# Optimization experiments

Hardware: AMD Instinct MI355X
Metric: run time of the kernel (lower is better)

The kernel has to match this reference:

```python
import jax, jax.numpy as jnp
import numpy as np

H, D_MODEL, D_K, D_V = 8, 512, 64, 64
B, S = 8, 2048


def setup_inputs() -> dict:
    key = jax.random.key(0)
    ks = jax.random.split(key, 11)
    scale = 1.0 / np.sqrt(D_MODEL)
    inp = {
        "q": jax.random.normal(ks[0], (B, S, D_MODEL), dtype=jnp.float32),
        "k": jax.random.normal(ks[1], (B, S, D_MODEL), dtype=jnp.float32),
        "v": jax.random.normal(ks[2], (B, S, D_MODEL), dtype=jnp.float32),
        # stacked per-head linear weights, [h, d_model, d_k/d_v] (in x out layout)
        "Wq": jax.random.normal(ks[3], (H, D_MODEL, D_K), dtype=jnp.float32) * scale,
        "bq": jax.random.normal(ks[4], (H, D_K), dtype=jnp.float32) * 0.01,
        "Wk": jax.random.normal(ks[5], (H, D_MODEL, D_K), dtype=jnp.float32) * scale,
        "bk": jax.random.normal(ks[6], (H, D_K), dtype=jnp.float32) * 0.01,
        "Wv": jax.random.normal(ks[7], (H, D_MODEL, D_V), dtype=jnp.float32) * scale,
        "bv": jax.random.normal(ks[8], (H, D_V), dtype=jnp.float32) * 0.01,
        "Wo": jax.random.normal(ks[9], (H * D_V, D_MODEL), dtype=jnp.float32) * (1.0 / np.sqrt(H * D_V)),
        "bo": jax.random.normal(ks[10], (D_MODEL,), dtype=jnp.float32) * 0.01,
    }
    return inp


def reference(q, k, v, Wq, bq, Wk, bk, Wv, bv, Wo, bo):
    # Per-head projections, vectorized over heads: [b, h, s, d_k]
    qh = jnp.einsum("bsd,hdk->bhsk", q, Wq) + bq[None, :, None, :]
    kh = jnp.einsum("bsd,hdk->bhsk", k, Wk) + bk[None, :, None, :]
    vh = jnp.einsum("bsd,hdv->bhsv", v, Wv) + bv[None, :, None, :]
    # scaled dot product: [b, h, s_q, s_k]
    scores = jnp.einsum("bhqd,bhkd->bhqk", qh, kh) / jnp.sqrt(jnp.float32(D_K))
    # NOTE: original applies softmax over dim=1 of [b, s_q, s_k] == the QUERY axis
    attn = jax.nn.softmax(scores, axis=2)
    ctx = jnp.einsum("bhqk,bhkv->bhqv", attn, vh)  # [b, h, s, d_v]
    # concat heads along feature dim (matches torch.cat(attentions, dim=2))
    concat = jnp.transpose(ctx, (0, 2, 1, 3)).reshape(ctx.shape[0], ctx.shape[2], H * D_V)
    return concat @ Wo + bo
```

## Files before the change

### kernel.cpp

```cpp
#include <hip/hip_runtime.h>
#include <hip/hip_bf16.h>
#include <math.h>

#define BB 8
#define SS 2048
#define HH 8
#define DM 512
#define DK 64

typedef short bf16x8 __attribute__((ext_vector_type(8)));
typedef float f32x4 __attribute__((ext_vector_type(4)));

static __device__ __forceinline__ short f2bf(float f) {
    union { __hip_bfloat16 h; short s; } u;
    u.h = __float2bfloat16(f);
    return u.s;
}

static __device__ __forceinline__ float fexp2(float x) {
#if __has_builtin(__builtin_amdgcn_exp2f)
    return __builtin_amdgcn_exp2f(x);
#else
    return __expf(x * 0.69314718056f);
#endif
}

static __device__ __forceinline__ void gld16(void* lds, const void* g) {
    __builtin_amdgcn_global_load_lds((const __attribute__((address_space(1))) void*)g,
                                     (__attribute__((address_space(3))) void*)lds, 16, 0, 0);
}

static __device__ __forceinline__ bf16x8 fragRow(const short* lds, int row, int cshort) {
    return *(const bf16x8*)(lds + row * 64 + (cshort ^ ((row & 7) << 3)));
}

static __device__ __forceinline__ void bar() {
    __builtin_amdgcn_s_barrier();
    __builtin_amdgcn_sched_barrier(0);
}
#define WAITV4 asm volatile("s_waitcnt vmcnt(4)" ::: "memory")
#define WAITV2 asm volatile("s_waitcnt vmcnt(2)" ::: "memory")
#define WAITV0 asm volatile("s_waitcnt vmcnt(0)" ::: "memory")
#define WAITL0 asm volatile("s_waitcnt lgkmcnt(0)" ::: "memory")
#define SCHED0 __builtin_amdgcn_sched_barrier(0)

__global__ __launch_bounds__(256) void tcvt(const float* __restrict__ src, short* __restrict__ dst,
                                            int R, int C) {
    __shared__ short T[64][72];
    const int r0 = blockIdx.x * 64, c0 = blockIdx.y * 64;
    const int t = threadIdx.x;
#pragma unroll
    for (int p = 0; p < 4; ++p) {
        int idx = t + 256 * p;
        int row = idx >> 4, c4 = (idx & 15) * 4;
        float4 v = *(const float4*)(src + (size_t)(r0 + row) * C + c0 + c4);
        T[c4 + 0][row] = f2bf(v.x);
        T[c4 + 1][row] = f2bf(v.y);
        T[c4 + 2][row] = f2bf(v.z);
        T[c4 + 3][row] = f2bf(v.w);
    }
    __syncthreads();
#pragma unroll
    for (int p = 0; p < 2; ++p) {
        int idx = t + 256 * p;
        int row = idx >> 3, slot = idx & 7;
        *(bf16x8*)(dst + (size_t)(c0 + row) * R + r0 + slot * 8) = *(const bf16x8*)&T[row][slot * 8];
    }
}

__global__ __launch_bounds__(256) void tcvt3(const float* __restrict__ Wq, const float* __restrict__ Wk,
                                             const float* __restrict__ Wv, short* __restrict__ WqT,
                                             short* __restrict__ WkT, short* __restrict__ WvT) {
    __shared__ short T[64][72];
    const int z = blockIdx.z;
    const int which = z >> 3, h = z & 7;
    const float* src = (which == 0 ? Wq : (which == 1 ? Wk : Wv)) + (size_t)h * DM * DK;
    short* dst = (which == 0 ? WqT : (which == 1 ? WkT : WvT)) + (size_t)h * DK * DM;
    const int r0 = blockIdx.x * 64;
    const int t = threadIdx.x;
#pragma unroll
    for (int p = 0; p < 4; ++p) {
        int idx = t + 256 * p;
        int row = idx >> 4, c4 = (idx & 15) * 4;
        float4 v = *(const float4*)(src + (size_t)(r0 + row) * DK + c4);
        T[c4 + 0][row] = f2bf(v.x);
        T[c4 + 1][row] = f2bf(v.y);
        T[c4 + 2][row] = f2bf(v.z);
        T[c4 + 3][row] = f2bf(v.w);
    }
    __syncthreads();
#pragma unroll
    for (int p = 0; p < 2; ++p) {
        int idx = t + 256 * p;
        int row = idx >> 3, slot = idx & 7;
        *(bf16x8*)(dst + (size_t)row * DM + r0 + slot * 8) = *(const bf16x8*)&T[row][slot * 8];
    }
}

__global__ __launch_bounds__(256, 4) void proj_mfma(const float* __restrict__ qX,
                                                    const float* __restrict__ kX,
                                                    const float* __restrict__ vX,
                                                    const short* __restrict__ WqT,
                                                    const short* __restrict__ WkT,
                                                    const short* __restrict__ WvT,
                                                    const float* __restrict__ bq,
                                                    const float* __restrict__ bk,
                                                    const float* __restrict__ bv,
                                                    short* __restrict__ qY,
                                                    short* __restrict__ kY,
                                                    short* __restrict__ vY,
                                                    float qscale) {
    __shared__ short As[128 * 64];
    __shared__ short Bs[2][64 * 64];
    const int mode = blockIdx.y;
    const float* X = mode == 0 ? qX : (mode == 1 ? kX : vX);
    const short* WT = mode == 0 ? WqT : (mode == 1 ? WkT : WvT);
    const float* bias = mode == 0 ? bq : (mode == 1 ? bk : bv);
    short* Y = mode == 0 ? qY : (mode == 1 ? kY : vY);
    const float scale = mode == 0 ? qscale : 1.0f;

    const int lin = blockIdx.x;
    const int b = lin & 7, h = (lin >> 3) & 7;
    const int s0 = (lin >> 6) * 128;
    const int bh = b * 8 + h;
    const int t = threadIdx.x;
    const int l = t & 63, w = t >> 6;
    const int lr = l & 15, g = l >> 4;
    const float* Xb = X + ((size_t)b * SS + s0) * DM;
    const short* Wh = WT + (size_t)h * DK * DM;
    f32x4 acc[2][4];
#pragma unroll
    for (int i = 0; i < 2; ++i)
#pragma unroll
        for (int j = 0; j < 4; ++j) acc[i][j] = (f32x4){0.f, 0.f, 0.f, 0.f};

    float4 ra[8];
    auto loadA = [&](int k0) {
#pragma unroll
        for (int p = 0; p < 4; ++p) {
            int c = p * 256 + t;
            int row = c >> 3, col = (c & 7) * 8;
            ra[2 * p]     = *(const float4*)(Xb + (size_t)row * DM + k0 + col);
            ra[2 * p + 1] = *(const float4*)(Xb + (size_t)row * DM + k0 + col + 4);
        }
    };
    auto writeA = [&]() {
#pragma unroll
        for (int p = 0; p < 4; ++p) {
            int c = p * 256 + t;
            int row = c >> 3, slot = c & 7;
            bf16x8 o;
            o[0] = f2bf(ra[2 * p].x); o[1] = f2bf(ra[2 * p].y);
            o[2] = f2bf(ra[2 * p].z); o[3] = f2bf(ra[2 * p].w);
            o[4] = f2bf(ra[2 * p + 1].x); o[5] = f2bf(ra[2 * p + 1].y);
            o[6] = f2bf(ra[2 * p + 1].z); o[7] = f2bf(ra[2 * p + 1].w);
            *(bf16x8*)(As + row * 64 + ((slot ^ (row & 7)) * 8)) = o;
        }
    };
    auto stageB = [&](int buf, int k0) {
#pragma unroll
        for (int p = 0; p < 2; ++p) {
            int c = p * 256 + w * 64 + l;
            int row = c >> 3, slot = c & 7;
            gld16(Bs[buf] + (size_t)(p * 256 + w * 64) * 8,
                  Wh + (size_t)row * DM + k0 + ((slot ^ (row & 7)) * 8));
        }
    };

    loadA(0);
    stageB(0, 0);
    writeA();
    __syncthreads();
    int cur = 0;
    for (int k0 = 0; k0 < DM; k0 += 64) {
        const bool next = (k0 + 64 < DM);
        if (next) { loadA(k0 + 64); stageB(cur ^ 1, k0 + 64); }
        SCHED0;
        bf16x8 bfr[4][2];
#pragma unroll
        for (int bf = 0; bf < 4; ++bf) {
            bfr[bf][0] = fragRow(Bs[cur], 16 * bf + lr, 8 * g);
            bfr[bf][1] = fragRow(Bs[cur], 16 * bf + lr, 32 + 8 * g);
        }
#pragma unroll
        for (int af = 0; af < 2; ++af) {
            bf16x8 a0 = fragRow(As, 32 * w + 16 * af + lr, 8 * g);
            bf16x8 a1 = fragRow(As, 32 * w + 16 * af + lr, 32 + 8 * g);
#pragma unroll
            for (int bf = 0; bf < 4; ++bf) {
                acc[af][bf] = __builtin_amdgcn_mfma_f32_16x16x32_bf16(a0, bfr[bf][0], acc[af][bf], 0, 0, 0);
                acc[af][bf] = __builtin_amdgcn_mfma_f32_16x16x32_bf16(a1, bfr[bf][1], acc[af][bf], 0, 0, 0);
            }
        }
        if (next) {
            bar();
            writeA();
            __syncthreads();
        }
        cur ^= 1;
    }
    if (mode == 2) {
        short* Yb = Y + (size_t)bh * DK * SS;
#pragma unroll
        for (int qf = 0; qf < 2; ++qf)
#pragma unroll
            for (int nf = 0; nf < 4; ++nf) {
                int n = 16 * nf + lr;
                float bv2 = bias[h * DK + n];
                short4 o;
                o.x = f2bf(acc[qf][nf][0] + bv2);
                o.y = f2bf(acc[qf][nf][1] + bv2);
                o.z = f2bf(acc[qf][nf][2] + bv2);
                o.w = f2bf(acc[qf][nf][3] + bv2);
                *(short4*)(Yb + (size_t)n * SS + s0 + 32 * w + 8 * g + 4 * qf) = o;
            }
    } else {
        short* Yb = Y + ((size_t)bh * SS + s0) * DK;
#pragma unroll
        for (int qf = 0; qf < 2; ++qf)
#pragma unroll
            for (int nf = 0; nf < 4; ++nf) {
                int n = 16 * nf + lr;
                float bv2 = bias[h * DK + n];
#pragma unroll
                for (int r = 0; r < 4; ++r)
                    Yb[(size_t)(32 * w + 16 * qf + 4 * g + r) * DK + n] =
                        f2bf((acc[qf][nf][r] + bv2) * scale);
            }
    }
}

__global__ __launch_bounds__(256, 4) void stats_mfma(const short* __restrict__ qs,
                                                     const short* __restrict__ kh,
                                                     float* __restrict__ izOut) {
    __shared__ short LDS[16384];
    const int bid = blockIdx.x;
    const int r = bid & 63;
    const int bh = ((r & 7) << 3) | (r >> 3);
    const int k0 = (bid >> 6) * 256;
    const int t = threadIdx.x;
    const int l = t & 63, w = t >> 6;
    const int lr = l & 15, g = l >> 4;
    const short* Qb = qs + (size_t)bh * SS * DK;
    const short* Kb = kh + ((size_t)bh * SS + k0) * DK;

#pragma unroll
    for (int p = 0; p < 8; ++p) {
        int c = p * 256 + w * 64 + l;
        int row = c >> 3, slot = c & 7;
        gld16(LDS + (size_t)(p * 256 + w * 64) * 8,
              Kb + (size_t)row * DK + ((slot ^ (row & 7)) * 8));
    }
    WAITV0;
    bar();
    bf16x8 bk[4][2];
#pragma unroll
    for (int c2 = 0; c2 < 4; ++c2) {
        bk[c2][0] = fragRow(LDS, 64 * w + 16 * c2 + lr, 8 * g);
        bk[c2][1] = fragRow(LDS, 64 * w + 16 * c2 + lr, 32 + 8 * g);
    }
    WAITL0;
    SCHED0;
    bar();

    auto stageQ = [&](int buf, int qq) {
#pragma unroll
        for (int p = 0; p < 2; ++p) {
            int c = p * 256 + w * 64 + l;
            int row = c >> 3, slot = c & 7;
            gld16(LDS + buf * 4096 + (size_t)(p * 256 + w * 64) * 8,
                  Qb + (size_t)(qq + row) * DK + ((slot ^ (row & 7)) * 8));
        }
    };
    stageQ(0, 0);
    stageQ(1, 64);
    WAITV2;
    bar();

    f32x4 zacc[4];
#pragma unroll
    for (int c2 = 0; c2 < 4; ++c2) zacc[c2] = (f32x4){0.f, 0.f, 0.f, 0.f};

    int cur = 0;
    for (int it = 0; it < 32; ++it) {
        const bool pre = (it < 30);
        if (pre) stageQ((cur + 2) & 3, (it + 2) * 64);
        const short* Qcur = LDS + cur * 4096;
        __builtin_amdgcn_s_setprio(1);
#pragma unroll
        for (int qf = 0; qf < 4; ++qf) {
            bf16x8 aq0 = fragRow(Qcur, 16 * qf + lr, 8 * g);
            bf16x8 aq1 = fragRow(Qcur, 16 * qf + lr, 32 + 8 * g);
#pragma unroll
            for (int c2 = 0; c2 < 4; ++c2) {
                f32x4 s = {0.f, 0.f, 0.f, 0.f};
                s = __builtin_amdgcn_mfma_f32_16x16x32_bf16(aq0, bk[c2][0], s, 0, 0, 0);
                s = __builtin_amdgcn_mfma_f32_16x16x32_bf16(aq1, bk[c2][1], s, 0, 0, 0);
#pragma unroll
                for (int rr = 0; rr < 4; ++rr)
                    zacc[c2][rr] += fexp2(s[rr]);
            }
        }
        __builtin_amdgcn_s_setprio(0);
        if (pre) { WAITV2; } else { WAITV0; }
        bar();
        cur = (cur + 1) & 3;
    }
#pragma unroll
    for (int c2 = 0; c2 < 4; ++c2) {
        float z = zacc[c2][0] + zacc[c2][1] + zacc[c2][2] + zacc[c2][3];
        z += __shfl_xor(z, 16);
        z += __shfl_xor(z, 32);
        if (l < 16)
            izOut[(size_t)bh * SS + k0 + 64 * w + 16 * c2 + l] = 1.f / z;
    }
}

__global__ __launch_bounds__(256, 2) void ctx_mfma(const short* __restrict__ qs,
                                                   const short* __restrict__ kh,
                                                   const short* __restrict__ vP,
                                                   const float* __restrict__ izArr,
                                                   short* __restrict__ ctxc) {
    __shared__ short LDS[24576];
    const int bid = blockIdx.x;
    const int r = bid & 63;
    const int bh = ((r & 7) << 3) | (r >> 3);
    const int q0 = (bid >> 6) * 256;
    const int b = bh >> 3, h = bh & 7;
    const int t = threadIdx.x;
    const int l = t & 63, w = t >> 6;
    const int lr = l & 15, g = l >> 4;
    const short* Qb = qs + ((size_t)bh * SS + q0) * DK;
    const short* Kb = kh + (size_t)bh * SS * DK;
    const short* Vb = vP + (size_t)bh * DK * SS;
    const float* zB = izArr + (size_t)bh * SS;

#pragma unroll
    for (int p = 0; p < 8; ++p) {
        int c = p * 256 + w * 64 + l;
        int row = c >> 3, slot = c & 7;
        gld16(LDS + (size_t)(p * 256 + w * 64) * 8,
              Qb + (size_t)row * DK + ((slot ^ (row & 7)) * 8));
    }
    WAITV0;
    bar();
    bf16x8 qfr[4][2];
#pragma unroll
    for (int qf = 0; qf < 4; ++qf)
#pragma unroll
        for (int c = 0; c < 2; ++c)
            qfr[qf][c] = fragRow(LDS, 64 * w + 16 * qf + lr, 32 * c + 8 * g);
    WAITL0;
    SCHED0;
    bar();

    auto stageKV = [&](int buf, int kk) {
#pragma unroll
        for (int p = 0; p < 2; ++p) {
            int c = p * 256 + w * 64 + l;
            int row = c >> 3, slot = c & 7;
            gld16(LDS + buf * 4096 + (size_t)(p * 256 + w * 64) * 8,
                  Kb + (size_t)(kk + row) * DK + ((slot ^ (row & 7)) * 8));
        }
#pragma unroll
        for (int p = 0; p < 2; ++p) {
            int c = p * 256 + w * 64 + l;
            int row = c >> 3, slot = c & 7;
            gld16(LDS + 12288 + buf * 4096 + (size_t)(p * 256 + w * 64) * 8,
                  Vb + (size_t)row * SS + kk + ((slot ^ (row & 7)) * 8));
        }
    };
    stageKV(0, 0);
    stageKV(1, 64);
    WAITV4;
    bar();

    f32x4 acc[4][4];
#pragma unroll
    for (int a = 0; a < 4; ++a)
#pragma unroll
        for (int b2 = 0; b2 < 4; ++b2) acc[a][b2] = (f32x4){0.f, 0.f, 0.f, 0.f};

    int cur = 0;
    for (int it = 0; it < 32; ++it) {
        const int k0 = it * 64;
        const bool pre = (it < 30);
        f32x4 z4[4];
#pragma unroll
        for (int kf = 0; kf < 4; ++kf)
            z4[kf] = *(const f32x4*)(zB + k0 + 16 * kf + 4 * g);
        SCHED0;
        if (pre) {
            int nb = cur + 2; if (nb >= 3) nb -= 3;
            stageKV(nb, k0 + 128);
        }
        const short* Kcur = LDS + cur * 4096;
        const short* Vcur = LDS + 12288 + cur * 4096;
        __builtin_amdgcn_s_setprio(1);
        bf16x8 Kf[4][2];
#pragma unroll
        for (int kf = 0; kf < 4; ++kf) {
            Kf[kf][0] = fragRow(Kcur, 16 * kf + lr, 8 * g);
            Kf[kf][1] = fragRow(Kcur, 16 * kf + lr, 32 + 8 * g);
        }
        bf16x8 pa[4][2];
#pragma unroll
        for (int qf = 0; qf < 4; ++qf) {
            float pw[4][4];
#pragma unroll
            for (int kf = 0; kf < 4; ++kf) {
                f32x4 s = {0.f, 0.f, 0.f, 0.f};
                s = __builtin_amdgcn_mfma_f32_16x16x32_bf16(Kf[kf][0], qfr[qf][0], s, 0, 0, 0);
                s = __builtin_amdgcn_mfma_f32_16x16x32_bf16(Kf[kf][1], qfr[qf][1], s, 0, 0, 0);
#pragma unroll
                for (int rr = 0; rr < 4; ++rr)
                    pw[kf][rr] = fexp2(s[rr]) * z4[kf][rr];
            }
#pragma unroll
            for (int c = 0; c < 2; ++c)
#pragma unroll
                for (int e = 0; e < 4; ++e) {
                    pa[qf][c][e]     = f2bf(pw[2 * c][e]);
                    pa[qf][c][4 + e] = f2bf(pw[2 * c + 1][e]);
                }
        }
#pragma unroll
        for (int vf = 0; vf < 4; ++vf)
#pragma unroll
            for (int c = 0; c < 2; ++c) {
                bf16x8 bv2 = fragRow(Vcur, 16 * vf + lr, 32 * c + 8 * g);
#pragma unroll
                for (int qf = 0; qf < 4; ++qf)
                    acc[qf][vf] = __builtin_amdgcn_mfma_f32_16x16x32_bf16(pa[qf][c], bv2, acc[qf][vf], 0, 0, 0);
            }
        __builtin_amdgcn_s_setprio(0);
        if (pre) { WAITV4; } else { WAITV0; }
        bar();
        cur = (cur == 2) ? 0 : cur + 1;
    }
    short* Cb = ctxc + ((size_t)b * SS + q0) * (HH * DK) + h * DK;
#pragma unroll
    for (int qf = 0; qf < 4; ++qf)
#pragma unroll
        for (int vf = 0; vf < 4; ++vf)
#pragma unroll
            for (int rr = 0; rr < 4; ++rr)
                Cb[(size_t)(64 * w + 16 * qf + 4 * g + rr) * (HH * DK) + 16 * vf + lr] =
                    f2bf(acc[qf][vf][rr]);
}

__global__ __launch_bounds__(256) void out_mfma(const short* __restrict__ A,
                                                const short* __restrict__ BT,
                                                const float* __restrict__ bo,
                                                float* __restrict__ out) {
    __shared__ short As[2][128 * 64];
    __shared__ short Bs[2][128 * 64];
    const int r0 = blockIdx.x * 128;
    const int j0 = blockIdx.y * 128;
    const int t = threadIdx.x;
    const int l = t & 63, w = t >> 6;
    const int lr = l & 15, g = l >> 4;
    const int wr = w >> 1, wc = w & 1;
    f32x4 acc[4][4];
#pragma unroll
    for (int i = 0; i < 4; ++i)
#pragma unroll
        for (int j = 0; j < 4; ++j) acc[i][j] = (f32x4){0.f, 0.f, 0.f, 0.f};

    auto stage = [&](int buf, int k0) {
#pragma unroll
        for (int p = 0; p < 4; ++p) {
            int c = p * 256 + w * 64 + l;
            int row = c >> 3, slot = c & 7;
            gld16(As[buf] + (size_t)(p * 256 + w * 64) * 8,
                  A + (size_t)(r0 + row) * DM + k0 + ((slot ^ (row & 7)) * 8));
            gld16(Bs[buf] + (size_t)(p * 256 + w * 64) * 8,
                  BT + (size_t)(j0 + row) * DM + k0 + ((slot ^ (row & 7)) * 8));
        }
    };
    stage(0, 0);
    WAITV0;
    __syncthreads();
    int cur = 0;
    for (int k0 = 0; k0 < DM; k0 += 64) {
        if (k0 + 64 < DM) stage(cur ^ 1, k0 + 64);
        bf16x8 bfr[4][2];
#pragma unroll
        for (int bf = 0; bf < 4; ++bf) {
            bfr[bf][0] = fragRow(Bs[cur], 64 * wc + 16 * bf + lr, 8 * g);
            bfr[bf][1] = fragRow(Bs[cur], 64 * wc + 16 * bf + lr, 32 + 8 * g);
        }
#pragma unroll
        for (int af = 0; af < 4; ++af) {
            bf16x8 a0 = fragRow(As[cur], 64 * wr + 16 * af + lr, 8 * g);
            bf16x8 a1 = fragRow(As[cur], 64 * wr + 16 * af + lr, 32 + 8 * g);
#pragma unroll
            for (int bf = 0; bf < 4; ++bf) {
                acc[af][bf] = __builtin_amdgcn_mfma_f32_16x16x32_bf16(a0, bfr[bf][0], acc[af][bf], 0, 0, 0);
                acc[af][bf] = __builtin_amdgcn_mfma_f32_16x16x32_bf16(a1, bfr[bf][1], acc[af][bf], 0, 0, 0);
            }
        }
        __syncthreads();
        cur ^= 1;
    }
#pragma unroll
    for (int af = 0; af < 4; ++af)
#pragma unroll
        for (int bf = 0; bf < 4; ++bf) {
            int j = j0 + 64 * wc + 16 * bf + lr;
            float bv2 = bo[j];
#pragma unroll
            for (int rr = 0; rr < 4; ++rr)
                out[(size_t)(r0 + 64 * wr + 16 * af + 4 * g + rr) * DM + j] = acc[af][bf][rr] + bv2;
        }
}

extern "C" void kernel_launch(void* const* d_in, const int* in_sizes, int n_in,
                              void* d_out, int out_size, void* d_ws, size_t ws_size,
                              hipStream_t stream) {
    const float* q  = (const float*)d_in[0];
    const float* k  = (const float*)d_in[1];
    const float* v  = (const float*)d_in[2];
    const float* Wq = (const float*)d_in[3];
    const float* bq = (const float*)d_in[4];
    const float* Wk = (const float*)d_in[5];
    const float* bk = (const float*)d_in[6];
    const float* Wv = (const float*)d_in[7];
    const float* bv = (const float*)d_in[8];
    const float* Wo = (const float*)d_in[9];
    const float* bo = (const float*)d_in[10];
    float* out = (float*)d_out;

    short* w16 = (short*)d_ws;
    const size_t NH = (size_t)BB * HH * SS * DK;
    const size_t NW = (size_t)HH * DM * DK;
    short* WqT = w16;
    short* WkT = WqT + NW;
    short* WvT = WkT + NW;
    short* WoT = WvT + NW;
    short* qsb = WoT + NW;
    short* khb = qsb + NH;
    short* vtb = khb + NH;
    short* ctc = vtb + NH;
    float* izb = (float*)(ctc + NH);

    const float qscale = 0.125f * 1.4426950408889634f;

    dim3 blk(256);
    tcvt3<<<dim3(8, 1, 24), blk, 0, stream>>>(Wq, Wk, Wv, WqT, WkT, WvT);
    tcvt<<<dim3(8, 8), blk, 0, stream>>>(Wo, WoT, DM, DM);
    proj_mfma<<<dim3(1024, 3), blk, 0, stream>>>(q, k, v, WqT, WkT, WvT, bq, bk, bv,
                                                 qsb, khb, vtb, qscale);
    stats_mfma<<<dim3(512), blk, 0, stream>>>(qsb, khb, izb);
    ctx_mfma<<<dim3(512), blk, 0, stream>>>(qsb, khb, vtb, izb, ctc);
    out_mfma<<<dim3(128, 4), blk, 0, stream>>>(ctc, WoT, bo, out);
}
```

Measured before the change: 191.6 us.

## Software-pipeline S computation one tile ahead with 4-deep K/V ring buffer

Restructures the ctx_mfma loop so the score MFMAs and exp for tile it+1 are issued before the P·V MFMAs for tile it. The bf16 probability fragments are double-buffered in registers (paA/paB), and the loop is unrolled by two. The K/V LDS ring grows from three to four stages, so LDS use goes from 48KB to 64KB per block. It also drops the s_setprio hints. The aim is to overlap exp/convert work with matrix ops and hide load latency, at the cost of more registers and LDS that may hurt occupancy at 2 blocks per CU.

```diff
diff --git a/kernel.cpp b/kernel.cpp
--- a/kernel.cpp
+++ b/kernel.cpp
@@ -321,7 +321,7 @@
                                                    const short* __restrict__ vP,
                                                    const float* __restrict__ izArr,
                                                    short* __restrict__ ctxc) {
-    __shared__ short LDS[24576];
+    __shared__ short LDS[32768];
     const int bid = blockIdx.x;
     const int r = bid & 63;
     const int bh = ((r & 7) << 3) | (r >> 3);
@@ -366,44 +366,20 @@
         for (int p = 0; p < 2; ++p) {
             int c = p * 256 + w * 64 + l;
             int row = c >> 3, slot = c & 7;
-            gld16(LDS + 12288 + buf * 4096 + (size_t)(p * 256 + w * 64) * 8,
+            gld16(LDS + 16384 + buf * 4096 + (size_t)(p * 256 + w * 64) * 8,
                   Vb + (size_t)row * SS + kk + ((slot ^ (row & 7)) * 8));
         }
     };
-    stageKV(0, 0);
-    stageKV(1, 64);
-    WAITV4;
-    bar();
-
-    f32x4 acc[4][4];
-#pragma unroll
-    for (int a = 0; a < 4; ++a)
-#pragma unroll
-        for (int b2 = 0; b2 < 4; ++b2) acc[a][b2] = (f32x4){0.f, 0.f, 0.f, 0.f};
-
-    int cur = 0;
-    for (int it = 0; it < 32; ++it) {
-        const int k0 = it * 64;
-        const bool pre = (it < 30);
-        f32x4 z4[4];
-#pragma unroll
-        for (int kf = 0; kf < 4; ++kf)
-            z4[kf] = *(const f32x4*)(zB + k0 + 16 * kf + 4 * g);
-        SCHED0;
-        if (pre) {
-            int nb = cur + 2; if (nb >= 3) nb -= 3;
-            stageKV(nb, k0 + 128);
-        }
-        const short* Kcur = LDS + cur * 4096;
-        const short* Vcur = LDS + 12288 + cur * 4096;
-        __builtin_amdgcn_s_setprio(1);
+
+    f32x4 zn[4];
+    auto computeS = [&](int bS, const f32x4 (&z4)[4], bf16x8 (&pa)[4][2]) {
+        const short* Kcur = LDS + bS * 4096;
         bf16x8 Kf[4][2];
 #pragma unroll
         for (int kf = 0; kf < 4; ++kf) {
             Kf[kf][0] = fragRow(Kcur, 16 * kf + lr, 8 * g);
             Kf[kf][1] = fragRow(Kcur, 16 * kf + lr, 32 + 8 * g);
         }
-        bf16x8 pa[4][2];
 #pragma unroll
         for (int qf = 0; qf < 4; ++qf) {
             float pw[4][4];
@@ -424,6 +400,34 @@
                     pa[qf][c][4 + e] = f2bf(pw[2 * c + 1][e]);
                 }
         }
+    };
+
+    f32x4 acc[4][4];
+#pragma unroll
+    for (int a = 0; a < 4; ++a)
+#pragma unroll
+        for (int b2 = 0; b2 < 4; ++b2) acc[a][b2] = (f32x4){0.f, 0.f, 0.f, 0.f};
+
+    bf16x8 paA[4][2], paB[4][2];
+    {
+        f32x4 z0[4];
+        stageKV(0, 0);
+#pragma unroll
+        for (int kf = 0; kf < 4; ++kf) z0[kf] = *(const f32x4*)(zB + 16 * kf + 4 * g);
+        SCHED0;
+        stageKV(1, 64);
+#pragma unroll
+        for (int kf = 0; kf < 4; ++kf) zn[kf] = *(const f32x4*)(zB + 64 + 16 * kf + 4 * g);
+        SCHED0;
+        stageKV(2, 128);
+        WAITV4;
+        bar();
+        computeS(0, z0, paA);
+    }
+
+    auto body = [&](int it, bf16x8 (&paC)[4][2], bf16x8 (&paN)[4][2]) {
+        if (it < 31) computeS((it + 1) & 3, zn, paN);
+        const short* Vcur = LDS + 16384 + (it & 3) * 4096;
 #pragma unroll
         for (int vf = 0; vf < 4; ++vf)
 #pragma unroll
@@ -431,13 +435,24 @@
                 bf16x8 bv2 = fragRow(Vcur, 16 * vf + lr, 32 * c + 8 * g);
 #pragma unroll
                 for (int qf = 0; qf < 4; ++qf)
-                    acc[qf][vf] = __builtin_amdgcn_mfma_f32_16x16x32_bf16(pa[qf][c], bv2, acc[qf][vf], 0, 0, 0);
-            }
-        __builtin_amdgcn_s_setprio(0);
-        if (pre) { WAITV4; } else { WAITV0; }
+                    acc[qf][vf] = __builtin_amdgcn_mfma_f32_16x16x32_bf16(paC[qf][c], bv2, acc[qf][vf], 0, 0, 0);
+            }
+        if (it < 30) {
+#pragma unroll
+            for (int kf = 0; kf < 4; ++kf)
+                zn[kf] = *(const f32x4*)(zB + (it + 2) * 64 + 16 * kf + 4 * g);
+        }
+        SCHED0;
+        if (it < 29) stageKV((it + 3) & 3, (it + 3) * 64);
+        if (it < 29) { WAITV4; } else { WAITV0; }
         bar();
-        cur = (cur == 2) ? 0 : cur + 1;
-    }
+    };
+
+    for (int it2 = 0; it2 < 32; it2 += 2) {
+        body(it2, paA, paB);
+        body(it2 + 1, paB, paA);
+    }
+
     short* Cb = ctxc + ((size_t)b * SS + q0) * (HH * DK) + h * DK;
 #pragma unroll
     for (int qf = 0; qf < 4; ++qf)
```

Measured after the change: 219.9 us. 14.8% more time.
